# Optimization experiments

Measured on AMD Instinct MI355X. Metric: run time of the kernel, lower is better.

## Reference

```python
import jax, jax.numpy as jnp
import numpy as np

B, H, SEQ, D = 2, 16, 4096, 64
WM = WN = 64
R = 3
NEG = -10000.0


def _forward(q, k, v, rand_attn, from_mask, to_mask, rand_mask, band_mask):
    b, h, m, d = q.shape
    n = k.shape[2]
    wm, wn, r = WM, WN, R
    scale = float(1.0 / np.sqrt(d))
    bq = q.reshape(b, h, m // wm, wm, d)
    bk = k.reshape(b, h, n // wn, wn, d)
    bv = v.reshape(b, h, n // wn, wn, d)
    nw = m // wm - 2  # non-global query blocks
    # gather random key/value blocks: [b,h,nw,r*wn,d]
    idx = rand_attn.reshape(b, h, nw * r)[:, :, :, None, None]
    gk = jnp.take_along_axis(bk, idx, axis=2).reshape(b, h, nw, r * wn, d)
    gv = jnp.take_along_axis(bv, idx, axis=2).reshape(b, h, nw, r * wn, d)

    # --- block 0: full (global) attention over all keys ---
    p1 = jnp.einsum('bhqd,bhkd->bhqk', bq[:, :, 0], k) * scale + (1.0 - to_mask) * NEG
    c1 = jnp.einsum('bhqk,bhkd->bhqd', jax.nn.softmax(p1, -1), v)[:, :, None]

    # --- block 1: blocks [0,1,2,last] + random blocks ---
    k2 = jnp.concatenate([bk[:, :, 0], bk[:, :, 1], bk[:, :, 2], bk[:, :, -1], gk[:, :, 0]], axis=2)
    v2 = jnp.concatenate([bv[:, :, 0], bv[:, :, 1], bv[:, :, 2], bv[:, :, -1], gv[:, :, 0]], axis=2)
    p2 = jnp.einsum('bhqd,bhkd->bhqk', bq[:, :, 1], k2) * scale
    seq_pad = jnp.concatenate([to_mask[:, :, :, :3 * wn], to_mask[:, :, :, -wn:],
                               jnp.ones((b, 1, 1, r * wn), to_mask.dtype)], axis=3)
    rand_pad = jnp.concatenate([jnp.ones((b, h, wm, 4 * wn), rand_mask.dtype), rand_mask[:, :, 0]], axis=3)
    p2 = p2 + (1.0 - jnp.minimum(seq_pad, rand_pad)) * NEG
    c2 = jnp.einsum('bhqk,bhkd->bhqd', jax.nn.softmax(p2, -1), v2)[:, :, None]

    # --- middle blocks 2..-3: sliding window + random + first/last global ---
    ek = jnp.concatenate([bk[:, :, 1:-3], bk[:, :, 2:-2], bk[:, :, 3:-1]], axis=3)
    ev = jnp.concatenate([bv[:, :, 1:-3], bv[:, :, 2:-2], bv[:, :, 3:-1]], axis=3)
    mq = bq[:, :, 2:-2]
    inner = jnp.einsum('bhlqd,bhlkd->bhlqk', mq, ek) * scale + (1.0 - band_mask) * NEG
    randp = jnp.einsum('bhlqd,bhlkd->bhlqk', mq, gk[:, :, 1:-1]) * scale + (1.0 - rand_mask[:, :, 1:-1]) * NEG
    firstp = jnp.einsum('bhlqd,bhkd->bhlqk', mq, bk[:, :, 0]) * scale + (1.0 - to_mask[:, :, :, None, :wn]) * NEG
    lastp = jnp.einsum('bhlqd,bhkd->bhlqk', mq, bk[:, :, -1]) * scale + (1.0 - to_mask[:, :, :, None, -wn:]) * NEG
    band = jnp.concatenate([firstp, inner, randp, lastp], axis=-1)  # [b,h,l,wm, wn+3wn+r*wn+wn]
    attn = jax.nn.softmax(band, -1)
    cm = jnp.einsum('bhlqk,bhlkd->bhlqd', attn[..., wn:4 * wn], ev)
    cm = cm + jnp.einsum('bhlqk,bhlkd->bhlqd', attn[..., 4 * wn:4 * wn + r * wn], gv[:, :, 1:-1])
    cm = cm + jnp.einsum('bhlqk,bhkd->bhlqd', attn[..., :wn], bv[:, :, 0])
    cm = cm + jnp.einsum('bhlqk,bhkd->bhlqd', attn[..., -wn:], bv[:, :, -1])

    # --- block -2: blocks [0,-3,-2,-1] + random blocks ---
    k3 = jnp.concatenate([bk[:, :, 0], bk[:, :, -3], bk[:, :, -2], bk[:, :, -1], gk[:, :, -1]], axis=2)
    v3 = jnp.concatenate([bv[:, :, 0], bv[:, :, -3], bv[:, :, -2], bv[:, :, -1], gv[:, :, -1]], axis=2)
    p3 = jnp.einsum('bhqd,bhkd->bhqk', bq[:, :, -2], k3) * scale
    seq_pad3 = jnp.concatenate([to_mask[:, :, :, :wn], to_mask[:, :, :, -3 * wn:],
                                jnp.ones((b, 1, 1, r * wn), to_mask.dtype)], axis=3)
    rand_pad3 = jnp.concatenate([jnp.ones((b, h, wm, 4 * wn), rand_mask.dtype), rand_mask[:, :, -1]], axis=3)
    p3 = p3 + (1.0 - jnp.minimum(seq_pad3, rand_pad3)) * NEG
    c3 = jnp.einsum('bhqk,bhkd->bhqd', jax.nn.softmax(p3, -1), v3)[:, :, None]

    # --- last block: full (global) attention ---
    p4 = jnp.einsum('bhqd,bhkd->bhqk', bq[:, :, -1], k) * scale + (1.0 - to_mask) * NEG
    c4 = jnp.einsum('bhqk,bhkd->bhqd', jax.nn.softmax(p4, -1), v)[:, :, None]

    ctx = jnp.concatenate([c1, c2, cm, c3, c4], axis=2).reshape(b, h, m, d)
    return ctx * from_mask


def setup_inputs() -> dict:
    key = jax.random.key(0)
    ks = jax.random.split(key, 4)
    nb = SEQ // WM
    return {
        'query_layer': jax.random.normal(ks[0], (B, H, SEQ, D), jnp.float32),
        'key_layer': jax.random.normal(ks[1], (B, H, SEQ, D), jnp.float32),
        'value_layer': jax.random.normal(ks[2], (B, H, SEQ, D), jnp.float32),
        'rand_attn': jax.random.randint(ks[3], (B, H, nb - 2, R), 0, nb),
        'from_mask': jnp.ones((B, 1, SEQ, 1), jnp.float32),
        'to_mask': jnp.ones((B, 1, 1, SEQ), jnp.float32),
        'rand_mask': jnp.ones((B, H, nb - 2, WM, R * WN), jnp.float32),
        'band_mask': jnp.ones((B, 1, nb - 4, WM, 3 * WN), jnp.float32),
        'batch_size': B,
        'from_seq_length': SEQ,
        'to_seq_length': SEQ,
    }


def reference(query_layer, key_layer, value_layer, rand_attn, from_mask, to_mask, rand_mask, band_mask, batch_size, from_seq_length, to_seq_length):
    return _forward(query_layer, key_layer, value_layer, rand_attn, from_mask, to_mask, rand_mask, band_mask)
```

## Files before the change

### kernel.cpp

```cpp
#include <hip/hip_runtime.h>
#include <hip/hip_bf16.h>

typedef short  short8  __attribute__((ext_vector_type(8)));
typedef float  float4v __attribute__((ext_vector_type(4)));
typedef int    int4v   __attribute__((ext_vector_type(4)));

#define SEQ    4096
#define DHEAD  64
#define NBLK   64
#define NCHUNK 8
#define CHK    8
#define WGPB   78
#define ENTRY_FLOATS 4160
#define KS_ELEMS (2L * 16 * 4096 * 64)

__device__ __forceinline__ short f2bf(float f) {
    unsigned u = __float_as_uint(f);
    u += 0x7fffu + ((u >> 16) & 1u);
    return (short)(u >> 16);
}

__device__ __forceinline__ unsigned cvt_pk_bf16(float lo, float hi) {
    unsigned r;
    asm("v_cvt_pk_bf16_f32 %0, %1, %2" : "=v"(r) : "v"(lo), "v"(hi));
    return r;
}

__device__ __forceinline__ void gload16(const void* g, void* l) {
    __builtin_amdgcn_global_load_lds(
        (const __attribute__((address_space(1))) unsigned int*)g,
        (__attribute__((address_space(3))) unsigned int*)l, 16, 0, 0);
}

__global__ __launch_bounds__(256)
void bigbird_prep(const float* __restrict__ K,
                  const float* __restrict__ V,
                  short* __restrict__ wsS) {
    __shared__ float tile[64 * 65];
    const int bh = blockIdx.x >> 6;
    const int kb = blockIdx.x & 63;
    const int t  = threadIdx.x;
    char* Ks = (char*)wsS;
    char* VT = (char*)(wsS + KS_ELEMS);
    const long blk_off = (long)(bh * 64 + kb) * 8192;

    const int row = t >> 2, seg = t & 3;
    const long gsrc = ((long)bh * SEQ + kb * 64 + row) * DHEAD + seg * 16;

    {
        const float* kp = K + gsrc;
        short8 s0, s1;
#pragma unroll
        for (int i = 0; i < 4; ++i) {
            float4v x = ((const float4v*)kp)[i];
#pragma unroll
            for (int jj = 0; jj < 4; ++jj) {
                short v = f2bf(x[jj]);
                if (i < 2) s0[i * 4 + jj] = v; else s1[(i - 2) * 4 + jj] = v;
            }
        }
        char* kbase = Ks + blk_off + (long)row * 128;
        const int sw = (row & 7) << 4;
        *(short8*)(kbase + ((seg * 32)      ^ sw)) = s0;
        *(short8*)(kbase + ((seg * 32 + 16) ^ sw)) = s1;
    }
    {
        const float* vp = V + gsrc;
#pragma unroll
        for (int i = 0; i < 4; ++i) {
            float4v x = ((const float4v*)vp)[i];
#pragma unroll
            for (int jj = 0; jj < 4; ++jj)
                tile[row * 65 + seg * 16 + i * 4 + jj] = x[jj];
        }
    }
    __syncthreads();
    {
        const int d = t >> 2, kk = t & 3;
        short8 s0, s1;
#pragma unroll
        for (int i = 0; i < 8; ++i) {
            s0[i] = f2bf(tile[(kk * 16 + i) * 65 + d]);
            s1[i] = f2bf(tile[(kk * 16 + 8 + i) * 65 + d]);
        }
        char* vbase = VT + blk_off + (long)d * 128;
        const int sw = (d & 7) << 4;
        *(short8*)(vbase + ((kk * 32)      ^ sw)) = s0;
        *(short8*)(vbase + ((kk * 32 + 16) ^ sw)) = s1;
    }
}

__global__ __launch_bounds__(256, 5)
void bigbird_main(const float* __restrict__ Q,
                  const int* __restrict__ rand_attn,
                  float* __restrict__ out,
                  const short* __restrict__ wsS,
                  float* __restrict__ part) {
    __shared__ short kb_s[2][4096];
    __shared__ short vt_s[2][4096];

    const int gi   = blockIdx.x;
    const int xcd  = gi & 7;
    const int slot = gi >> 3;
    const int bh   = xcd + 8 * (slot / WGPB);
    const int j    = slot % WGPB;
    const bool split = (j >= 62);
    int qb, chunk = 0, nk;
    if (!split) { qb = j + 1; nk = (qb == 1 || qb == 62) ? 7 : 8; }
    else        { int s2 = j - 62; qb = (s2 >> 3) ? 63 : 0; chunk = s2 & 7; nk = CHK; }

    const int tid  = threadIdx.x;
    const int wave = tid >> 6;
    const int lane = tid & 63;
    const int l15  = lane & 15;
    const int quad = lane >> 4;

    const long base = (long)bh * SEQ * DHEAD;
    const char* Ksb = (const char*)wsS + (long)bh * (NBLK * 8192);
    const char* VTb = (const char*)(wsS + KS_ELEMS) + (long)bh * (NBLK * 8192);

    int rnd0 = 0, rnd1 = 0, rnd2 = 0;
    if (!split) {
        const int rbase = (bh * 62 + (qb - 1)) * 3;
        rnd0 = rand_attn[rbase + 0];
        rnd1 = rand_attn[rbase + 1];
        rnd2 = rand_attn[rbase + 2];
    }
    auto kb_of = [&](int it) -> int {
        if (split) return chunk * CHK + it;
        const int nband = (qb == 1 || qb == 62) ? 4 : 5;
        if (it >= nband) {
            const int ir = it - nband;
            return ir == 0 ? rnd0 : ir == 1 ? rnd1 : rnd2;
        }
        if (qb == 1)  return it <= 2 ? it : 63;
        if (qb == 62) return it == 0 ? 0 : 60 + it;
        return it == 0 ? 0 : it <= 3 ? qb - 2 + it : 63;
    };

    short8 aq0, aq1;
    {
        const float* qp = Q + base + (long)(qb * 64 + wave * 16 + l15) * DHEAD + quad * 8;
        float4v x0 = *(const float4v*)(qp);
        float4v x1 = *(const float4v*)(qp + 4);
        float4v x2 = *(const float4v*)(qp + 32);
        float4v x3 = *(const float4v*)(qp + 36);
#pragma unroll
        for (int i = 0; i < 4; ++i) {
            aq0[i]     = f2bf(0.125f * x0[i]);
            aq0[4 + i] = f2bf(0.125f * x1[i]);
            aq1[i]     = f2bf(0.125f * x2[i]);
            aq1[4 + i] = f2bf(0.125f * x3[i]);
        }
    }

    auto stage = [&](int kb, int buf) {
        const char* kg = Ksb + (long)kb * 8192;
        const char* vg = VTb + (long)kb * 8192;
        char* kd = (char*)kb_s[buf];
        char* vd = (char*)vt_s[buf];
        const int off = tid * 16;
        gload16(kg + off,        kd + off);
        gload16(kg + 4096 + off, kd + 4096 + off);
        gload16(vg + off,        vd + off);
        gload16(vg + 4096 + off, vd + 4096 + off);
    };

    float4v o[4];
#pragma unroll
    for (int nt = 0; nt < 4; ++nt) o[nt] = (float4v)0.0f;
    float l_acc = 0.0f;

    stage(kb_of(0), 0);
    __syncthreads();

    for (int it = 0; it < nk; ++it) {
        const int cur = it & 1;
        if (it + 1 < nk)
            stage(kb_of(it + 1), cur ^ 1);

        float4v p[4];
#pragma unroll
        for (int nt = 0; nt < 4; ++nt) {
            const int rr = nt * 16 + l15;
            const char* kro = (const char*)kb_s[cur] + rr * 128;
            const int sw = (rr & 7) << 4;
            short8 b0 = *(const short8*)(kro + ((quad * 16)      ^ sw));
            short8 b1 = *(const short8*)(kro + ((64 + quad * 16) ^ sw));
            float4v acc = (float4v)0.0f;
            acc = __builtin_amdgcn_mfma_f32_16x16x32_bf16(b0, aq0, acc, 0, 0, 0);
            acc = __builtin_amdgcn_mfma_f32_16x16x32_bf16(b1, aq1, acc, 0, 0, 0);
            p[nt] = acc;
        }

#pragma unroll
        for (int nt = 0; nt < 4; ++nt) {
#pragma unroll
            for (int r = 0; r < 4; ++r) p[nt][r] = __expf(p[nt][r]);
        }
        l_acc += ((p[0][0] + p[0][1]) + (p[0][2] + p[0][3]))
               + ((p[1][0] + p[1][1]) + (p[1][2] + p[1][3]))
               + ((p[2][0] + p[2][1]) + (p[2][2] + p[2][3]))
               + ((p[3][0] + p[3][1]) + (p[3][2] + p[3][3]));

#pragma unroll
        for (int f = 0; f < 2; ++f) {
            unsigned x0 = cvt_pk_bf16(p[2 * f][0],     p[2 * f][1]);
            unsigned x1 = cvt_pk_bf16(p[2 * f][2],     p[2 * f][3]);
            unsigned y0 = cvt_pk_bf16(p[2 * f + 1][0], p[2 * f + 1][1]);
            unsigned y1 = cvt_pk_bf16(p[2 * f + 1][2], p[2 * f + 1][3]);
            asm("v_permlane32_swap_b32 %0, %1" : "+v"(x0), "+v"(y0));
            asm("v_permlane32_swap_b32 %0, %1" : "+v"(x1), "+v"(y1));
            asm("v_permlane16_swap_b32 %0, %1" : "+v"(x0), "+v"(y0));
            asm("v_permlane16_swap_b32 %0, %1" : "+v"(x1), "+v"(y1));
            int4v wi; wi[0] = (int)x0; wi[1] = (int)x1; wi[2] = (int)y0; wi[3] = (int)y1;
            union { int4v i; short8 s; } pu; pu.i = wi;
            const short8 pf = pu.s;
#pragma unroll
            for (int nt = 0; nt < 4; ++nt) {
                const int rr = nt * 16 + l15;
                const char* vro = (const char*)vt_s[cur] + rr * 128;
                const int sw = (rr & 7) << 4;
                short8 bv = *(const short8*)(vro + ((f * 64 + quad * 16) ^ sw));
                o[nt] = __builtin_amdgcn_mfma_f32_16x16x32_bf16(bv, pf, o[nt], 0, 0, 0);
            }
        }
        __syncthreads();
    }

    l_acc += __shfl_xor(l_acc, 16, 64);
    l_acc += __shfl_xor(l_acc, 32, 64);

    if (!split) {
        const float inv = 1.0f / l_acc;
        float* op = out + base + (long)(qb * 64 + wave * 16 + l15) * DHEAD;
#pragma unroll
        for (int nt = 0; nt < 4; ++nt) {
            float4v vv;
#pragma unroll
            for (int r = 0; r < 4; ++r) vv[r] = o[nt][r] * inv;
            *(float4v*)(op + nt * 16 + quad * 4) = vv;
        }
    } else {
        float* wsp = part + (long)((bh * 2 + (qb == 63)) * NCHUNK + chunk) * ENTRY_FLOATS;
        if (quad == 0) wsp[wave * 16 + l15] = l_acc;
        float* orow = wsp + 64 + (long)(wave * 16 + l15) * 64;
#pragma unroll
        for (int nt = 0; nt < 4; ++nt) {
            float4v vv;
#pragma unroll
            for (int r = 0; r < 4; ++r) vv[r] = o[nt][r];
            *(float4v*)(orow + nt * 16 + quad * 4) = vv;
        }
    }
}

__global__ __launch_bounds__(256)
void bigbird_combine(const float* __restrict__ part, float* __restrict__ out) {
    const int gid = blockIdx.x * 256 + threadIdx.x;
    const int dim = gid & 63;
    const int row = (gid >> 6) & 63;
    const int sel = (gid >> 12) & 1;
    const int bh  = gid >> 13;

    float num = 0.0f, den = 0.0f;
#pragma unroll
    for (int c = 0; c < NCHUNK; ++c) {
        const float* e = part + (long)((bh * 2 + sel) * NCHUNK + c) * ENTRY_FLOATS;
        den += e[row];
        num += e[64 + row * 64 + dim];
    }
    const int qb = sel ? 63 : 0;
    out[((long)bh * SEQ + qb * 64 + row) * DHEAD + dim] = num / den;
}

extern "C" void kernel_launch(void* const* d_in, const int* in_sizes, int n_in,
                              void* d_out, int out_size, void* d_ws, size_t ws_size,
                              hipStream_t stream) {
    const float* Q       = (const float*)d_in[0];
    const float* K       = (const float*)d_in[1];
    const float* V       = (const float*)d_in[2];
    const int* rand_attn = (const int*)d_in[3];
    float* out           = (float*)d_out;
    short* wsS           = (short*)d_ws;
    float* part          = (float*)((char*)d_ws + 2L * KS_ELEMS * sizeof(short));

    const int B = 2, H = 16;
    bigbird_prep<<<dim3(B * H * NBLK), dim3(256), 0, stream>>>(K, V, wsS);
    bigbird_main<<<dim3(B * H * WGPB), dim3(256), 0, stream>>>(Q, rand_attn, out, wsS, part);
    bigbird_combine<<<dim3((B * H * 2 * 64 * 64) / 256), dim3(256), 0, stream>>>(part, out);
}
```

Before: 264.0 us.

## Process two adjacent query blocks per workgroup to share staged K/V tiles

Each main-kernel workgroup now handles a pair of adjacent query blocks, each with its own accumulators. A per-iteration schedule stages the union of their key blocks once and applies each tile to one or both queries through a mask. The global blocks 0 and 63 share one split chunk pass. This roughly halves the workgroup count and the LDS staging traffic for shared band and global keys, at the cost of more registers (launch bounds drop from 5 to 4 waves) and less parallelism. The prep kernel's block-to-XCD mapping is also changed to group heads per XCD for L2 locality.

```diff
diff --git a/kernel.cpp b/kernel.cpp
--- a/kernel.cpp
+++ b/kernel.cpp
@@ -9,8 +9,7 @@
 #define DHEAD  64
 #define NBLK   64
 #define NCHUNK 8
-#define CHK    8
-#define WGPB   78
+#define WGPB   39
 #define ENTRY_FLOATS 4160
 #define KS_ELEMS (2L * 16 * 4096 * 64)
 
@@ -37,8 +36,11 @@
                   const float* __restrict__ V,
                   short* __restrict__ wsS) {
     __shared__ float tile[64 * 65];
-    const int bh = blockIdx.x >> 6;
-    const int kb = blockIdx.x & 63;
+    const int gi   = blockIdx.x;
+    const int xcd  = gi & 7;
+    const int slot = gi >> 3;
+    const int bh   = xcd + 8 * (slot >> 6);
+    const int kb   = slot & 63;
     const int t  = threadIdx.x;
     char* Ks = (char*)wsS;
     char* VT = (char*)(wsS + KS_ELEMS);
@@ -90,7 +92,7 @@
     }
 }
 
-__global__ __launch_bounds__(256, 5)
+__global__ __launch_bounds__(256, 4)
 void bigbird_main(const float* __restrict__ Q,
                   const int* __restrict__ rand_attn,
                   float* __restrict__ out,
@@ -104,10 +106,14 @@
     const int slot = gi >> 3;
     const int bh   = xcd + 8 * (slot / WGPB);
     const int j    = slot % WGPB;
-    const bool split = (j >= 62);
-    int qb, chunk = 0, nk;
-    if (!split) { qb = j + 1; nk = (qb == 1 || qb == 62) ? 7 : 8; }
-    else        { int s2 = j - 62; qb = (s2 >> 3) ? 63 : 0; chunk = s2 & 7; nk = CHK; }
+    const bool split = (j >= 31);
+    int qb1, qb2, chunk = 0, nk;
+    if (!split) {
+        qb1 = 2 * j + 1; qb2 = 2 * j + 2;
+        nk = (j == 0 || j == 30) ? 11 : 12;
+    } else {
+        chunk = j - 31; qb1 = 0; qb2 = 63; nk = 8;
+    }
 
     const int tid  = threadIdx.x;
     const int wave = tid >> 6;
@@ -119,38 +125,51 @@
     const char* Ksb = (const char*)wsS + (long)bh * (NBLK * 8192);
     const char* VTb = (const char*)(wsS + KS_ELEMS) + (long)bh * (NBLK * 8192);
 
-    int rnd0 = 0, rnd1 = 0, rnd2 = 0;
+    int r1a = 0, r1b = 0, r1c = 0, r2a = 0, r2b = 0, r2c = 0;
     if (!split) {
-        const int rbase = (bh * 62 + (qb - 1)) * 3;
-        rnd0 = rand_attn[rbase + 0];
-        rnd1 = rand_attn[rbase + 1];
-        rnd2 = rand_attn[rbase + 2];
-    }
-    auto kb_of = [&](int it) -> int {
-        if (split) return chunk * CHK + it;
-        const int nband = (qb == 1 || qb == 62) ? 4 : 5;
-        if (it >= nband) {
-            const int ir = it - nband;
-            return ir == 0 ? rnd0 : ir == 1 ? rnd1 : rnd2;
-        }
-        if (qb == 1)  return it <= 2 ? it : 63;
-        if (qb == 62) return it == 0 ? 0 : 60 + it;
-        return it == 0 ? 0 : it <= 3 ? qb - 2 + it : 63;
+        const int rbase = (bh * 62 + (qb1 - 1)) * 3;
+        r1a = rand_attn[rbase + 0]; r1b = rand_attn[rbase + 1]; r1c = rand_attn[rbase + 2];
+        r2a = rand_attn[rbase + 3]; r2b = rand_attn[rbase + 4]; r2c = rand_attn[rbase + 5];
+    }
+    auto sched = [&](int it, int& kb, int& m) {
+        if (split) { kb = chunk * 8 + it; m = 3; return; }
+        if (j == 0) {
+            if (it <= 3)      { kb = it; m = (it == 3) ? 2 : 3; }
+            else if (it == 4) { kb = 63; m = 3; }
+            else if (it <= 7) { kb = it == 5 ? r1a : it == 6 ? r1b : r1c; m = 1; }
+            else              { kb = it == 8 ? r2a : it == 9 ? r2b : r2c; m = 2; }
+        } else if (j == 30) {
+            if (it == 0)      { kb = 0; m = 3; }
+            else if (it <= 3) { kb = 59 + it; m = (it == 1) ? 1 : 3; }
+            else if (it == 4) { kb = 63; m = 3; }
+            else if (it <= 7) { kb = it == 5 ? r1a : it == 6 ? r1b : r1c; m = 1; }
+            else              { kb = it == 8 ? r2a : it == 9 ? r2b : r2c; m = 2; }
+        } else {
+            if (it == 0)      { kb = 0; m = 3; }
+            else if (it == 1) { kb = qb1 - 1; m = 1; }
+            else if (it == 2) { kb = qb1; m = 3; }
+            else if (it == 3) { kb = qb2; m = 3; }
+            else if (it == 4) { kb = qb2 + 1; m = 2; }
+            else if (it == 5) { kb = 63; m = 3; }
+            else if (it <= 8) { kb = it == 6 ? r1a : it == 7 ? r1b : r1c; m = 1; }
+            else              { kb = it == 9 ? r2a : it == 10 ? r2b : r2c; m = 2; }
+        }
     };
 
-    short8 aq0, aq1;
+    short8 aq10, aq11, aq20, aq21;
     {
-        const float* qp = Q + base + (long)(qb * 64 + wave * 16 + l15) * DHEAD + quad * 8;
-        float4v x0 = *(const float4v*)(qp);
-        float4v x1 = *(const float4v*)(qp + 4);
-        float4v x2 = *(const float4v*)(qp + 32);
-        float4v x3 = *(const float4v*)(qp + 36);
+        const float* qp1 = Q + base + (long)(qb1 * 64 + wave * 16 + l15) * DHEAD + quad * 8;
+        const float* qp2 = Q + base + (long)(qb2 * 64 + wave * 16 + l15) * DHEAD + quad * 8;
+        float4v a0 = *(const float4v*)(qp1),      a1 = *(const float4v*)(qp1 + 4);
+        float4v a2 = *(const float4v*)(qp1 + 32), a3 = *(const float4v*)(qp1 + 36);
+        float4v b0 = *(const float4v*)(qp2),      b1 = *(const float4v*)(qp2 + 4);
+        float4v b2 = *(const float4v*)(qp2 + 32), b3 = *(const float4v*)(qp2 + 36);
 #pragma unroll
         for (int i = 0; i < 4; ++i) {
-            aq0[i]     = f2bf(0.125f * x0[i]);
-            aq0[4 + i] = f2bf(0.125f * x1[i]);
-            aq1[i]     = f2bf(0.125f * x2[i]);
-            aq1[4 + i] = f2bf(0.125f * x3[i]);
+            aq10[i] = f2bf(0.125f * a0[i]); aq10[4 + i] = f2bf(0.125f * a1[i]);
+            aq11[i] = f2bf(0.125f * a2[i]); aq11[4 + i] = f2bf(0.125f * a3[i]);
+            aq20[i] = f2bf(0.125f * b0[i]); aq20[4 + i] = f2bf(0.125f * b1[i]);
+            aq21[i] = f2bf(0.125f * b2[i]); aq21[4 + i] = f2bf(0.125f * b3[i]);
         }
     }
 
@@ -166,19 +185,8 @@
         gload16(vg + 4096 + off, vd + 4096 + off);
     };
 
-    float4v o[4];
-#pragma unroll
-    for (int nt = 0; nt < 4; ++nt) o[nt] = (float4v)0.0f;
-    float l_acc = 0.0f;
-
-    stage(kb_of(0), 0);
-    __syncthreads();
-
-    for (int it = 0; it < nk; ++it) {
-        const int cur = it & 1;
-        if (it + 1 < nk)
-            stage(kb_of(it + 1), cur ^ 1);
-
+    auto tile_step = [&](int cur, const short8& aqA, const short8& aqB,
+                         float4v (&o)[4], float& l) {
         float4v p[4];
 #pragma unroll
         for (int nt = 0; nt < 4; ++nt) {
@@ -188,21 +196,19 @@
             short8 b0 = *(const short8*)(kro + ((quad * 16)      ^ sw));
             short8 b1 = *(const short8*)(kro + ((64 + quad * 16) ^ sw));
             float4v acc = (float4v)0.0f;
-            acc = __builtin_amdgcn_mfma_f32_16x16x32_bf16(b0, aq0, acc, 0, 0, 0);
-            acc = __builtin_amdgcn_mfma_f32_16x16x32_bf16(b1, aq1, acc, 0, 0, 0);
+            acc = __builtin_amdgcn_mfma_f32_16x16x32_bf16(b0, aqA, acc, 0, 0, 0);
+            acc = __builtin_amdgcn_mfma_f32_16x16x32_bf16(b1, aqB, acc, 0, 0, 0);
             p[nt] = acc;
         }
-
 #pragma unroll
         for (int nt = 0; nt < 4; ++nt) {
 #pragma unroll
             for (int r = 0; r < 4; ++r) p[nt][r] = __expf(p[nt][r]);
         }
-        l_acc += ((p[0][0] + p[0][1]) + (p[0][2] + p[0][3]))
-               + ((p[1][0] + p[1][1]) + (p[1][2] + p[1][3]))
-               + ((p[2][0] + p[2][1]) + (p[2][2] + p[2][3]))
-               + ((p[3][0] + p[3][1]) + (p[3][2] + p[3][3]));
-
+        l += ((p[0][0] + p[0][1]) + (p[0][2] + p[0][3]))
+           + ((p[1][0] + p[1][1]) + (p[1][2] + p[1][3]))
+           + ((p[2][0] + p[2][1]) + (p[2][2] + p[2][3]))
+           + ((p[3][0] + p[3][1]) + (p[3][2] + p[3][3]));
 #pragma unroll
         for (int f = 0; f < 2; ++f) {
             unsigned x0 = cvt_pk_bf16(p[2 * f][0],     p[2 * f][1]);
@@ -225,32 +231,55 @@
                 o[nt] = __builtin_amdgcn_mfma_f32_16x16x32_bf16(bv, pf, o[nt], 0, 0, 0);
             }
         }
+    };
+
+    float4v o1[4], o2[4];
+#pragma unroll
+    for (int nt = 0; nt < 4; ++nt) { o1[nt] = (float4v)0.0f; o2[nt] = (float4v)0.0f; }
+    float l1 = 0.0f, l2 = 0.0f;
+
+    { int kb0_, m0_; sched(0, kb0_, m0_); stage(kb0_, 0); }
+    __syncthreads();
+
+    for (int it = 0; it < nk; ++it) {
+        const int cur = it & 1;
+        int kb_c, m_c; sched(it, kb_c, m_c);
+        if (it + 1 < nk) { int kbN, mN; sched(it + 1, kbN, mN); stage(kbN, cur ^ 1); }
+
+        if (m_c & 1) tile_step(cur, aq10, aq11, o1, l1);
+        if (m_c & 2) tile_step(cur, aq20, aq21, o2, l2);
+
         __syncthreads();
     }
 
-    l_acc += __shfl_xor(l_acc, 16, 64);
-    l_acc += __shfl_xor(l_acc, 32, 64);
+    l1 += __shfl_xor(l1, 16, 64); l1 += __shfl_xor(l1, 32, 64);
+    l2 += __shfl_xor(l2, 16, 64); l2 += __shfl_xor(l2, 32, 64);
 
     if (!split) {
-        const float inv = 1.0f / l_acc;
-        float* op = out + base + (long)(qb * 64 + wave * 16 + l15) * DHEAD;
+        const float i1 = 1.0f / l1, i2 = 1.0f / l2;
+        float* op1 = out + base + (long)(qb1 * 64 + wave * 16 + l15) * DHEAD;
+        float* op2 = out + base + (long)(qb2 * 64 + wave * 16 + l15) * DHEAD;
 #pragma unroll
         for (int nt = 0; nt < 4; ++nt) {
-            float4v vv;
-#pragma unroll
-            for (int r = 0; r < 4; ++r) vv[r] = o[nt][r] * inv;
-            *(float4v*)(op + nt * 16 + quad * 4) = vv;
+            float4v v1, v2;
+#pragma unroll
+            for (int r = 0; r < 4; ++r) { v1[r] = o1[nt][r] * i1; v2[r] = o2[nt][r] * i2; }
+            *(float4v*)(op1 + nt * 16 + quad * 4) = v1;
+            *(float4v*)(op2 + nt * 16 + quad * 4) = v2;
         }
     } else {
-        float* wsp = part + (long)((bh * 2 + (qb == 63)) * NCHUNK + chunk) * ENTRY_FLOATS;
-        if (quad == 0) wsp[wave * 16 + l15] = l_acc;
-        float* orow = wsp + 64 + (long)(wave * 16 + l15) * 64;
+        float* w1 = part + (long)((bh * 2 + 0) * NCHUNK + chunk) * ENTRY_FLOATS;
+        float* w2 = part + (long)((bh * 2 + 1) * NCHUNK + chunk) * ENTRY_FLOATS;
+        if (quad == 0) { w1[wave * 16 + l15] = l1; w2[wave * 16 + l15] = l2; }
+        float* o1r = w1 + 64 + (long)(wave * 16 + l15) * 64;
+        float* o2r = w2 + 64 + (long)(wave * 16 + l15) * 64;
 #pragma unroll
         for (int nt = 0; nt < 4; ++nt) {
-            float4v vv;
-#pragma unroll
-            for (int r = 0; r < 4; ++r) vv[r] = o[nt][r];
-            *(float4v*)(orow + nt * 16 + quad * 4) = vv;
+            float4v v1, v2;
+#pragma unroll
+            for (int r = 0; r < 4; ++r) { v1[r] = o1[nt][r]; v2[r] = o2[nt][r]; }
+            *(float4v*)(o1r + nt * 16 + quad * 4) = v1;
+            *(float4v*)(o2r + nt * 16 + quad * 4) = v2;
         }
     }
 }
```

Measured after the change: 329.2 us. 24.7% more time.
